# Kernel optimization log

Hardware: AMD Instinct MI355X
Metric: run time of the kernel (lower is better)

## Reference

```python
import jax, jax.numpy as jnp
import numpy as np

H = 768  # hidden size
L = 2    # num layers


def _lstm_layer(xs, ms, Wih, Whh, bih, bhh):
    """xs: [S,B,in], ms: [S,B,H] mask. Returns (outputs [S,B,H], (hT, cT)).
    PyTorch LSTMCell gate order: i, f, g, o. Zero initial state (module default),
    so the reset term init_hidden*(1-mask) is identically zero."""
    B = xs.shape[1]
    h0 = jnp.zeros((B, H), xs.dtype)
    c0 = jnp.zeros((B, H), xs.dtype)
    # Precompute input projections for all timesteps in one big GEMM.
    x_proj = jnp.einsum('sbi,gi->sbg', xs, Wih) + bih + bhh  # [S,B,4H]

    def step(carry, inp):
        h, c = carry
        xp, mt = inp
        gates = xp + h @ Whh.T  # [B,4H]
        i, f, g, o = jnp.split(gates, 4, axis=-1)
        i = jax.nn.sigmoid(i)
        f = jax.nn.sigmoid(f)
        g = jnp.tanh(g)
        o = jax.nn.sigmoid(o)
        c_next = (f * c + i * g)
        h_next = o * jnp.tanh(c_next)
        # mask-based state reset (h0=c0=0 -> pure multiply)
        h_next = h_next * mt
        c_next = c_next * mt
        return (h_next, c_next), h_next

    (hT, cT), outs = jax.lax.scan(step, (h0, c0), (x_proj, ms))
    return outs, (hT, cT)


def setup_inputs() -> dict:
    key = jax.random.key(0)
    ks = jax.random.split(key, 5)
    s = 0.05
    return {
        'x': jax.random.normal(ks[0], (64, 512, 768), jnp.float32),
        'mask': jnp.ones((64, 512), jnp.float32),
        'W_ih': jax.random.normal(ks[1], (L, 4 * H, 768), jnp.float32) * s,
        'W_hh': jax.random.normal(ks[2], (L, 4 * H, H), jnp.float32) * s,
        'b_ih': jax.random.normal(ks[3], (L, 4 * H), jnp.float32) * s,
        'b_hh': jax.random.normal(ks[4], (L, 4 * H), jnp.float32) * s,
    }


def reference(x, mask, W_ih, W_hh, b_ih, b_hh):
    # batch_first=True: transpose to [S,B,...]
    xs = jnp.transpose(x, (1, 0, 2))          # [S,B,in]
    ms = jnp.transpose(mask, (1, 0))[:, :, None]  # [S,B,1]
    ms = jnp.broadcast_to(ms, ms.shape[:2] + (H,))  # [S,B,H]
    hn, cn = [], []
    inp = xs
    for l in range(L):
        outs, (hT, cT) = _lstm_layer(inp, ms, W_ih[l], W_hh[l], b_ih[l], b_hh[l])
        hn.append(hT)
        cn.append(cT)
        inp = outs
    output = jnp.transpose(inp, (1, 0, 2))  # [B,S,H]
    return output, (jnp.stack(hn, 0), jnp.stack(cn, 0))
```

## Files before the change

### kernel.cpp

```cpp
#include <hip/hip_runtime.h>
#include <hip/hip_bf16.h>


#define HID 768
#define FH  3072
#define SEQ 512
#define BAT 64
#define GB  16
#define WPG 64
#define CPW 12
#define NWG 256
#define TPB 768

typedef __attribute__((ext_vector_type(8))) __bf16 bf16x8;
typedef __attribute__((ext_vector_type(4))) float f32x4;
typedef unsigned int u32;

__device__ __forceinline__ float sigm(float z) { return 1.f / (1.f + __expf(-z)); }
__device__ __forceinline__ float tanh_fast(float x) {
  float a = fabsf(x);
  float e = __expf(-2.f * a);
  float t = (1.f - e) / (1.f + e);
  return copysignf(t, x);
}
__device__ __forceinline__ unsigned short bfbits(__bf16 b) {
  union { __bf16 b; unsigned short s; } u; u.b = b; return u.s;
}
__device__ __forceinline__ __bf16 bits2bf(unsigned short s) {
  union { unsigned short s; __bf16 b; } u; u.s = s; return u.b;
}
__device__ __forceinline__ u32 packsplit(float v) {
  __bf16 h = (__bf16)v;
  __bf16 l = (__bf16)(v - (float)h);
  return ((u32)bfbits(h) << 16) | (u32)bfbits(l);
}
__device__ __forceinline__ void split8(const float* p, bf16x8& hi, bf16x8& lo) {
  const float4* q = (const float4*)p;
  float4 a = q[0], b = q[1];
  float v[8] = {a.x, a.y, a.z, a.w, b.x, b.y, b.z, b.w};
#pragma unroll
  for (int i = 0; i < 8; ++i) {
    __bf16 h = (__bf16)v[i];
    hi[i] = h;
    lo[i] = (__bf16)(v[i] - (float)h);
  }
}
__device__ __forceinline__ void unpack8(const u32 w[8], bf16x8& hi, bf16x8& lo) {
#pragma unroll
  for (int i = 0; i < 8; ++i) {
    hi[i] = bits2bf((unsigned short)(w[i] >> 16));
    lo[i] = bits2bf((unsigned short)(w[i] & 0xffffu));
  }
}

template<int FMT>
__device__ __forceinline__ f32x4 proj384(const float* xf, const u32* xp,
                                         size_t base,
                                         const bf16x8* ah, const bf16x8* al) {
  f32x4 acc[4];
#pragma unroll
  for (int r = 0; r < 4; ++r) acc[r] = f32x4{0.f, 0.f, 0.f, 0.f};
#pragma unroll
  for (int kk = 0; kk < 12; ++kk) {
    bf16x8 bhi, blo;
    if constexpr (FMT == 0) {
      split8(xf + base + kk*32, bhi, blo);
    } else {
      const uint4* p = (const uint4*)(xp + base + kk*32);
      uint4 A = p[0], B = p[1];
      u32 w[8] = {A.x, A.y, A.z, A.w, B.x, B.y, B.z, B.w};
      unpack8(w, bhi, blo);
    }
    acc[(3*kk+0)&3] = __builtin_amdgcn_mfma_f32_16x16x32_bf16(ah[kk], bhi, acc[(3*kk+0)&3], 0, 0, 0);
    acc[(3*kk+1)&3] = __builtin_amdgcn_mfma_f32_16x16x32_bf16(al[kk], bhi, acc[(3*kk+1)&3], 0, 0, 0);
    acc[(3*kk+2)&3] = __builtin_amdgcn_mfma_f32_16x16x32_bf16(ah[kk], blo, acc[(3*kk+2)&3], 0, 0, 0);
  }
  return acc[0] + acc[1] + acc[2] + acc[3];
}

template<int XFMT, int WRITE_OUT>
__global__ void __launch_bounds__(TPB)
__attribute__((amdgpu_waves_per_eu(3, 3)))
lstm_scan(const float* __restrict__ xf,
          const u32* __restrict__ xp,
          const float* __restrict__ mask,
          const float* __restrict__ Wih,
          const float* __restrict__ Whh,
          const float* __restrict__ bih,
          const float* __restrict__ bhh,
          u32* __restrict__ hstream,
          float* __restrict__ out_f,
          float* __restrict__ hn,
          float* __restrict__ cn,
          int* __restrict__ flags)
{
  __shared__ f32x4 xacc_l[4][3][64];
  __shared__ f32x4 xpart_l[3][64];
  __shared__ f32x4 hpart_l[2][3][64];

  const int wg  = blockIdx.x;
  const int grp = wg >> 6;
  const int wid = wg & 63;
  const int tid = threadIdx.x;
  const int wv  = tid >> 6;
  const int l   = tid & 63;
  const int l15 = l & 15;
  const int lhi = l >> 4;

  const bool isx  = (wv < 6);
  const int lane6 = isx ? wv : (wv - 6);
  const int tile  = lane6 >> 1;
  const int half  = lane6 & 1;
  const int kofs  = half * 384;

  const int colA = wid*CPW + tile*4 + (l15 >> 2);
  const int qA   = l15 & 3;
  const float* wrow = (isx ? Wih : Whh) + (size_t)(qA*HID + colA)*HID + kofs + lhi*8;
  bf16x8 ah[12], al[12];
#pragma unroll
  for (int kk = 0; kk < 12; ++kk) split8(wrow + kk*32, ah[kk], al[kk]);

  const int batch = grp*GB + l15;
  const int colO  = wid*CPW + tile*4 + lhi;
  float bias4[4] = {0.f, 0.f, 0.f, 0.f};
  if (!isx && half == 1) {
#pragma unroll
    for (int j = 0; j < 4; ++j) bias4[j] = bih[j*HID + colO] + bhh[j*HID + colO];
  }
  const float* mrow = mask + batch*SEQ;
  int* gflags = flags + grp*WPG;

  const int kb = kofs + lhi*8;

  float cstate = 0.f;

  {
    f32x4 px{0.f, 0.f, 0.f, 0.f};
    if (isx) {
      size_t base = (XFMT == 0) ? ((size_t)batch*SEQ)*HID + kb
                                : ((size_t)batch)*HID + kb;
      px = proj384<XFMT>(xf, xp, base, ah, al);
      if (half == 0) xpart_l[tile][l] = px;
    }
    __syncthreads();
    if (isx && half == 1) {
      f32x4 t = xpart_l[tile][l];
      xacc_l[0][tile][l] = px + t;
    }
    __syncthreads();
  }

#pragma unroll 1
  for (int s = 0; s < SEQ; ++s) {
    f32x4 xa{0.f, 0.f, 0.f, 0.f};
    if (isx && s + 1 < SEQ) {
      size_t base = (XFMT == 0) ? ((size_t)batch*SEQ + (s+1))*HID + kb
                                : ((size_t)(s+1)*BAT + batch)*HID + kb;
      xa = proj384<XFMT>(xf, xp, base, ah, al);
      if (half == 0) xpart_l[tile][l] = xa;
    }
    if (!isx && lane6 == 0 && s > 0) {
      while (true) {
        int v = __hip_atomic_load(gflags + l, __ATOMIC_RELAXED, __HIP_MEMORY_SCOPE_AGENT);
        if (__all(v >= s)) break;
        __builtin_amdgcn_s_sleep(1);
      }
    }
    __syncthreads();

    f32x4 ha{0.f, 0.f, 0.f, 0.f};
    if (!isx && s > 0) {
      size_t base = ((size_t)(s-1)*BAT + batch)*HID + kb;
      ha = proj384<1>(nullptr, hstream, base, ah, al);
      if (half == 0) hpart_l[s & 1][tile][l] = ha;
    }
    if (isx && half == 1 && s + 1 < SEQ) {
      f32x4 t = xpart_l[tile][l];
      xacc_l[(s+1) & 3][tile][l] = xa + t;
    }
    __syncthreads();

    if (!isx && half == 1) {
      f32x4 z = xacc_l[s & 3][tile][l];
      if (s > 0) { f32x4 hp = hpart_l[s & 1][tile][l]; z = z + ha + hp; }
      float zi = z[0] + bias4[0], zf = z[1] + bias4[1];
      float zg = z[2] + bias4[2], zo = z[3] + bias4[3];
      float iv = sigm(zi), fv = sigm(zf), gv = tanh_fast(zg), ov = sigm(zo);
      float c  = fv*cstate + iv*gv;
      float hv = ov * tanh_fast(c);
      float m  = mrow[s];
      hv *= m; c *= m; cstate = c;

      u32 hw = packsplit(hv);
      __hip_atomic_store(hstream + ((size_t)s*BAT + batch)*HID + colO, hw,
                         __ATOMIC_RELAXED, __HIP_MEMORY_SCOPE_AGENT);
      if constexpr (WRITE_OUT) {
        __builtin_nontemporal_store(hv, out_f + ((size_t)batch*SEQ + s)*HID + colO);
      }
      if (s == SEQ - 1) {
        hn[batch*HID + colO] = hv;
        cn[batch*HID + colO] = c;
      }
      asm volatile("s_waitcnt vmcnt(0)" ::: "memory");
    }
    __syncthreads();
    if (tid == 0)
      __hip_atomic_store(gflags + wid, s + 1,
                         __ATOMIC_RELAXED, __HIP_MEMORY_SCOPE_AGENT);
  }
}

extern "C" void kernel_launch(void* const* d_in, const int* in_sizes, int n_in,
                              void* d_out, int out_size, void* d_ws, size_t ws_size,
                              hipStream_t stream) {
  const float* x    = (const float*)d_in[0];
  const float* mask = (const float*)d_in[1];
  const float* Wih  = (const float*)d_in[2];
  const float* Whh  = (const float*)d_in[3];
  const float* bih  = (const float*)d_in[4];
  const float* bhh  = (const float*)d_in[5];
  float* out = (float*)d_out;

  char* ws = (char*)d_ws;
  const size_t STREAM_B = (size_t)SEQ * BAT * HID * sizeof(u32);
  u32* opk   = (u32*)(ws);
  u32* hpk   = (u32*)(ws + STREAM_B);
  int* flags = (int*)(ws + 2*STREAM_B);

  (void)hipMemsetAsync(flags, 0, 2*NWG*sizeof(int), stream);

  float* hn = out + 25165824;
  float* cn = out + 25165824 + 98304;

  lstm_scan<0, 0><<<dim3(NWG), dim3(TPB), 0, stream>>>(
      x, nullptr, mask, Wih, Whh, bih, bhh,
      opk, nullptr, hn, cn, flags);

  lstm_scan<1, 1><<<dim3(NWG), dim3(TPB), 0, stream>>>(
      nullptr, opk, mask,
      Wih + (size_t)FH*HID, Whh + (size_t)FH*HID, bih + FH, bhh + FH,
      hpk, out, hn + 49152, cn + 49152, flags + NWG);
}
```

Baseline: 11.80 ms.

## Stream prepacked weights from memory, use per-step counters and LDS-staged hidden ring

Weights are prepacked into a bf16 hi/lo MFMA fragment layout by a separate kernel and read from global/L2 on every step instead of being held in registers, and the waves_per_eu pin is dropped. Inter-workgroup sync changes from polling 64 per-workgroup flags to one per-step counter per batch group, bumped once all three h-tiles of a workgroup finish. The previous hidden state moves through a 2-slot global ring and is staged once into padded LDS, so each wave no longer loads it from the full stream. This cuts sync latency and register pressure but adds weight re-reads every step, which may slow the MFMA inner loop.

```diff
diff --git a/kernel.cpp b/kernel.cpp
--- a/kernel.cpp
+++ b/kernel.cpp
@@ -11,10 +11,13 @@
 #define CPW 12
 #define NWG 256
 #define TPB 768
+#define LROW 772
+#define WBLK (12*64*8)
 
 typedef __attribute__((ext_vector_type(8))) __bf16 bf16x8;
 typedef __attribute__((ext_vector_type(4))) float f32x4;
 typedef unsigned int u32;
+typedef unsigned long long u64;
 
 __device__ __forceinline__ float sigm(float z) { return 1.f / (1.f + __expf(-z)); }
 __device__ __forceinline__ float tanh_fast(float x) {
@@ -52,16 +55,49 @@
     lo[i] = bits2bf((unsigned short)(w[i] & 0xffffu));
   }
 }
+__device__ __forceinline__ bf16x8 q2b(uint4 q) {
+  union { uint4 q; bf16x8 v; } u; u.q = q; return u.v;
+}
+__device__ __forceinline__ uint4 b2q(bf16x8 v) {
+  union { bf16x8 v; uint4 q; } u; u.v = v; return u.q;
+}
+
+__global__ void pack_w(const float* __restrict__ Wih,
+                       const float* __restrict__ Whh,
+                       u32* __restrict__ wpk) {
+  const int NT = 2*2*64*6*12*64;
+  int t = blockIdx.x * blockDim.x + threadIdx.x;
+  if (t >= NT) return;
+  int lane = t & 63; int r = t >> 6;
+  int kk = r % 12;  r /= 12;
+  int lane6 = r % 6; r /= 6;
+  int wid = r % 64; r /= 64;
+  int proj = r & 1; int layer = r >> 1;
+  int tile = lane6 >> 1, half = lane6 & 1;
+  int l15 = lane & 15, lhi = lane >> 4;
+  int colA = wid*CPW + tile*4 + (l15 >> 2);
+  int qA   = l15 & 3;
+  int row  = qA*HID + colA;
+  int k    = half*384 + kk*32 + lhi*8;
+  const float* W = (proj == 0 ? Wih : Whh) + (size_t)layer*FH*HID;
+  bf16x8 hi, lo;
+  split8(W + (size_t)row*HID + k, hi, lo);
+  u32* dst = wpk + (size_t)t * 8;
+  *(uint4*)dst       = b2q(hi);
+  *(uint4*)(dst + 4) = b2q(lo);
+}
 
 template<int FMT>
-__device__ __forceinline__ f32x4 proj384(const float* xf, const u32* xp,
-                                         size_t base,
-                                         const bf16x8* ah, const bf16x8* al) {
+__device__ __forceinline__ f32x4 projW(const float* xf, const u32* xp,
+                                       size_t base, const u32* wb, int l) {
   f32x4 acc[4];
 #pragma unroll
   for (int r = 0; r < 4; ++r) acc[r] = f32x4{0.f, 0.f, 0.f, 0.f};
 #pragma unroll
   for (int kk = 0; kk < 12; ++kk) {
+    const uint4* wp = (const uint4*)(wb + (size_t)(kk*64 + l)*8);
+    bf16x8 Ah = q2b(wp[0]);
+    bf16x8 Al = q2b(wp[1]);
     bf16x8 bhi, blo;
     if constexpr (FMT == 0) {
       split8(xf + base + kk*32, bhi, blo);
@@ -71,32 +107,33 @@
       u32 w[8] = {A.x, A.y, A.z, A.w, B.x, B.y, B.z, B.w};
       unpack8(w, bhi, blo);
     }
-    acc[(3*kk+0)&3] = __builtin_amdgcn_mfma_f32_16x16x32_bf16(ah[kk], bhi, acc[(3*kk+0)&3], 0, 0, 0);
-    acc[(3*kk+1)&3] = __builtin_amdgcn_mfma_f32_16x16x32_bf16(al[kk], bhi, acc[(3*kk+1)&3], 0, 0, 0);
-    acc[(3*kk+2)&3] = __builtin_amdgcn_mfma_f32_16x16x32_bf16(ah[kk], blo, acc[(3*kk+2)&3], 0, 0, 0);
+    acc[(3*kk+0)&3] = __builtin_amdgcn_mfma_f32_16x16x32_bf16(Ah, bhi, acc[(3*kk+0)&3], 0, 0, 0);
+    acc[(3*kk+1)&3] = __builtin_amdgcn_mfma_f32_16x16x32_bf16(Al, bhi, acc[(3*kk+1)&3], 0, 0, 0);
+    acc[(3*kk+2)&3] = __builtin_amdgcn_mfma_f32_16x16x32_bf16(Ah, blo, acc[(3*kk+2)&3], 0, 0, 0);
   }
   return acc[0] + acc[1] + acc[2] + acc[3];
 }
 
 template<int XFMT, int WRITE_OUT>
 __global__ void __launch_bounds__(TPB)
-__attribute__((amdgpu_waves_per_eu(3, 3)))
 lstm_scan(const float* __restrict__ xf,
           const u32* __restrict__ xp,
           const float* __restrict__ mask,
-          const float* __restrict__ Wih,
-          const float* __restrict__ Whh,
+          const u32* __restrict__ wpk,
           const float* __restrict__ bih,
           const float* __restrict__ bhh,
           u32* __restrict__ hstream,
+          u32* __restrict__ ring,
           float* __restrict__ out_f,
           float* __restrict__ hn,
           float* __restrict__ cn,
-          int* __restrict__ flags)
+          int* __restrict__ cnt)
 {
+  __shared__ u32 hbuf[16 * LROW];
   __shared__ f32x4 xacc_l[4][3][64];
   __shared__ f32x4 xpart_l[3][64];
   __shared__ f32x4 hpart_l[2][3][64];
+  __shared__ int lctr[SEQ];
 
   const int wg  = blockIdx.x;
   const int grp = wg >> 6;
@@ -113,12 +150,7 @@
   const int half  = lane6 & 1;
   const int kofs  = half * 384;
 
-  const int colA = wid*CPW + tile*4 + (l15 >> 2);
-  const int qA   = l15 & 3;
-  const float* wrow = (isx ? Wih : Whh) + (size_t)(qA*HID + colA)*HID + kofs + lhi*8;
-  bf16x8 ah[12], al[12];
-#pragma unroll
-  for (int kk = 0; kk < 12; ++kk) split8(wrow + kk*32, ah[kk], al[kk]);
+  const u32* wbase = wpk + ((size_t)((isx ? 0 : 1)*64 + wid)*6 + lane6) * WBLK;
 
   const int batch = grp*GB + l15;
   const int colO  = wid*CPW + tile*4 + lhi;
@@ -128,9 +160,10 @@
     for (int j = 0; j < 4; ++j) bias4[j] = bih[j*HID + colO] + bhh[j*HID + colO];
   }
   const float* mrow = mask + batch*SEQ;
-  int* gflags = flags + grp*WPG;
-
+  int* cntg = cnt + grp*SEQ;
   const int kb = kofs + lhi*8;
+
+  for (int i = tid; i < SEQ; i += TPB) lctr[i] = 0;
 
   float cstate = 0.f;
 
@@ -139,50 +172,71 @@
     if (isx) {
       size_t base = (XFMT == 0) ? ((size_t)batch*SEQ)*HID + kb
                                 : ((size_t)batch)*HID + kb;
-      px = proj384<XFMT>(xf, xp, base, ah, al);
+      px = projW<XFMT>(xf, xp, base, wbase, l);
       if (half == 0) xpart_l[tile][l] = px;
     }
     __syncthreads();
-    if (isx && half == 1) {
-      f32x4 t = xpart_l[tile][l];
-      xacc_l[0][tile][l] = px + t;
-    }
+    if (isx && half == 1) xacc_l[0][tile][l] = px + xpart_l[tile][l];
     __syncthreads();
   }
 
 #pragma unroll 1
   for (int s = 0; s < SEQ; ++s) {
     f32x4 xa{0.f, 0.f, 0.f, 0.f};
-    if (isx && s + 1 < SEQ) {
-      size_t base = (XFMT == 0) ? ((size_t)batch*SEQ + (s+1))*HID + kb
-                                : ((size_t)(s+1)*BAT + batch)*HID + kb;
-      xa = proj384<XFMT>(xf, xp, base, ah, al);
-      if (half == 0) xpart_l[tile][l] = xa;
-    }
-    if (!isx && lane6 == 0 && s > 0) {
-      while (true) {
-        int v = __hip_atomic_load(gflags + l, __ATOMIC_RELAXED, __HIP_MEMORY_SCOPE_AGENT);
-        if (__all(v >= s)) break;
+    if (isx) {
+      if (s + 1 < SEQ) {
+        size_t base = (XFMT == 0) ? ((size_t)batch*SEQ + (s+1))*HID + kb
+                                  : ((size_t)(s+1)*BAT + batch)*HID + kb;
+        xa = projW<XFMT>(xf, xp, base, wbase, l);
+        if (half == 0) xpart_l[tile][l] = xa;
+      }
+    } else if (half == 0 && s > 0) {
+      const int* cp = cntg + (s - 1);
+      while (__hip_atomic_load(cp, __ATOMIC_RELAXED, __HIP_MEMORY_SCOPE_AGENT) < 64)
         __builtin_amdgcn_s_sleep(1);
+      const u32* rsrc = ring + (size_t)(((s-1) & 1)*BAT + grp*GB)*HID;
+      const int hlid = tile*64 + l;
+#pragma unroll
+      for (int i = 0; i < 16; ++i) {
+        const u64* sp = (const u64*)(rsrc + (size_t)i*HID + hlid*4);
+        u64 a = __hip_atomic_load(sp,     __ATOMIC_RELAXED, __HIP_MEMORY_SCOPE_AGENT);
+        u64 b = __hip_atomic_load(sp + 1, __ATOMIC_RELAXED, __HIP_MEMORY_SCOPE_AGENT);
+        *(uint4*)&hbuf[i*LROW + hlid*4] =
+            make_uint4((u32)a, (u32)(a >> 32), (u32)b, (u32)(b >> 32));
       }
     }
     __syncthreads();
 
     f32x4 ha{0.f, 0.f, 0.f, 0.f};
     if (!isx && s > 0) {
-      size_t base = ((size_t)(s-1)*BAT + batch)*HID + kb;
-      ha = proj384<1>(nullptr, hstream, base, ah, al);
+      f32x4 acc[4];
+#pragma unroll
+      for (int r = 0; r < 4; ++r) acc[r] = f32x4{0.f, 0.f, 0.f, 0.f};
+#pragma unroll
+      for (int kk = 0; kk < 12; ++kk) {
+        const uint4* wp = (const uint4*)(wbase + (size_t)(kk*64 + l)*8);
+        bf16x8 Ah = q2b(wp[0]);
+        bf16x8 Al = q2b(wp[1]);
+        int hb = l15*LROW + kofs + kk*32 + lhi*8;
+        uint4 qa = *(const uint4*)&hbuf[hb];
+        uint4 qb = *(const uint4*)&hbuf[hb + 4];
+        u32 w[8] = {qa.x, qa.y, qa.z, qa.w, qb.x, qb.y, qb.z, qb.w};
+        bf16x8 bhi, blo;
+        unpack8(w, bhi, blo);
+        acc[(3*kk+0)&3] = __builtin_amdgcn_mfma_f32_16x16x32_bf16(Ah, bhi, acc[(3*kk+0)&3], 0, 0, 0);
+        acc[(3*kk+1)&3] = __builtin_amdgcn_mfma_f32_16x16x32_bf16(Al, bhi, acc[(3*kk+1)&3], 0, 0, 0);
+        acc[(3*kk+2)&3] = __builtin_amdgcn_mfma_f32_16x16x32_bf16(Ah, blo, acc[(3*kk+2)&3], 0, 0, 0);
+      }
+      ha = acc[0] + acc[1] + acc[2] + acc[3];
       if (half == 0) hpart_l[s & 1][tile][l] = ha;
     }
-    if (isx && half == 1 && s + 1 < SEQ) {
-      f32x4 t = xpart_l[tile][l];
-      xacc_l[(s+1) & 3][tile][l] = xa + t;
-    }
+    if (isx && half == 1 && s + 1 < SEQ)
+      xacc_l[(s+1) & 3][tile][l] = xa + xpart_l[tile][l];
     __syncthreads();
 
     if (!isx && half == 1) {
       f32x4 z = xacc_l[s & 3][tile][l];
-      if (s > 0) { f32x4 hp = hpart_l[s & 1][tile][l]; z = z + ha + hp; }
+      if (s > 0) z = z + ha + hpart_l[s & 1][tile][l];
       float zi = z[0] + bias4[0], zf = z[1] + bias4[1];
       float zg = z[2] + bias4[2], zo = z[3] + bias4[3];
       float iv = sigm(zi), fv = sigm(zf), gv = tanh_fast(zg), ov = sigm(zo);
@@ -192,9 +246,11 @@
       hv *= m; c *= m; cstate = c;
 
       u32 hw = packsplit(hv);
-      __hip_atomic_store(hstream + ((size_t)s*BAT + batch)*HID + colO, hw,
+      __hip_atomic_store(ring + ((size_t)(s & 1)*BAT + batch)*HID + colO, hw,
                          __ATOMIC_RELAXED, __HIP_MEMORY_SCOPE_AGENT);
-      if constexpr (WRITE_OUT) {
+      if constexpr (!WRITE_OUT) {
+        __builtin_nontemporal_store(hw, hstream + ((size_t)s*BAT + batch)*HID + colO);
+      } else {
         __builtin_nontemporal_store(hv, out_f + ((size_t)batch*SEQ + s)*HID + colO);
       }
       if (s == SEQ - 1) {
@@ -202,11 +258,12 @@
         cn[batch*HID + colO] = c;
       }
       asm volatile("s_waitcnt vmcnt(0)" ::: "memory");
-    }
-    __syncthreads();
-    if (tid == 0)
-      __hip_atomic_store(gflags + wid, s + 1,
-                         __ATOMIC_RELAXED, __HIP_MEMORY_SCOPE_AGENT);
+      if (l == 0) {
+        int old = atomicAdd(&lctr[s], 1);
+        if (old == 2)
+          __hip_atomic_fetch_add(cntg + s, 1, __ATOMIC_RELAXED, __HIP_MEMORY_SCOPE_AGENT);
+      }
+    }
   }
 }
 
@@ -222,22 +279,27 @@
   float* out = (float*)d_out;
 
   char* ws = (char*)d_ws;
-  const size_t STREAM_B = (size_t)SEQ * BAT * HID * sizeof(u32);
-  u32* opk   = (u32*)(ws);
-  u32* hpk   = (u32*)(ws + STREAM_B);
-  int* flags = (int*)(ws + 2*STREAM_B);
-
-  (void)hipMemsetAsync(flags, 0, 2*NWG*sizeof(int), stream);
+  const size_t WPK_B = (size_t)2*2*64*6*12*64*8 * 4;
+  const size_t H0_B  = (size_t)SEQ*BAT*HID*4;
+  const size_t RING_B = (size_t)2*BAT*HID*4;
+  u32* wpk  = (u32*)ws;
+  u32* h0pk = (u32*)(ws + WPK_B);
+  u32* ring = (u32*)(ws + WPK_B + H0_B);
+  int* cnt  = (int*)(ws + WPK_B + H0_B + RING_B);
+
+  (void)hipMemsetAsync(cnt, 0, 2*4*SEQ*sizeof(int), stream);
+  pack_w<<<4608, 256, 0, stream>>>(Wih, Whh, wpk);
 
   float* hn = out + 25165824;
   float* cn = out + 25165824 + 98304;
 
+  const size_t WLAYER = (size_t)2*64*6*WBLK;
+
   lstm_scan<0, 0><<<dim3(NWG), dim3(TPB), 0, stream>>>(
-      x, nullptr, mask, Wih, Whh, bih, bhh,
-      opk, nullptr, hn, cn, flags);
+      x, nullptr, mask, wpk, bih, bhh,
+      h0pk, ring, nullptr, hn, cn, cnt);
 
   lstm_scan<1, 1><<<dim3(NWG), dim3(TPB), 0, stream>>>(
-      nullptr, opk, mask,
-      Wih + (size_t)FH*HID, Whh + (size_t)FH*HID, bih + FH, bhh + FH,
-      hpk, out, hn + 49152, cn + 49152, flags + NWG);
-}
+      nullptr, h0pk, mask, wpk + WLAYER, bih + FH, bhh + FH,
+      nullptr, ring, out, hn + 49152, cn + 49152, cnt + 4*SEQ);
+}
```

New measurement: 23.86 ms. 2.02x slower.
